# Optimization experiments

Hardware: AMD Instinct MI355X
Metric: run time of the kernel (lower is better)

Reference implementation:

```python
import jax, jax.numpy as jnp
import numpy as np
from jax import lax

NR, NC, DI, DO = 2048, 10, 8, 16  # routes, digit caps, in-dim, out-dim

# (t1, a1, b1, a2, b2, t3, a3, b3, a4, b4) piecewise-affine squash constants
PRIM_CONSTS = (-13.46416092, 0.000242759, 0.024488359, 0.002769205, 0.06089699,
               13.23405266, -0.002828244, 0.061313814, -0.000219038, 0.023874787)
DIGIT_CONSTS = (-0.075410217, -0.074520095, 0.349297946, -0.534473989, 0.27196494,
                0.062207676, 0.637642944, 0.295330779, 0.169344703, 0.353784456)


def _piecewise(s, t1, a1, b1, a2, b2, t3, a3, b3, a4, b4):
    # Faithful to the torch loop: new_sorted aliases sorted, so each segment
    # count (i1,i2,i3) is computed on the PARTIALLY-MODIFIED array, and each
    # slice end is idx-1 (off-by-one in the source), last slice ends at n-1.
    n = s.shape[0]
    ar = jnp.arange(n)
    i1 = jnp.sum(s < t1)
    s = jnp.where(ar < i1 - 1, a1 * s + b1, s)
    i2 = jnp.sum(s < 0.0)
    s = jnp.where((ar >= i1) & (ar < i2 - 1), a2 * s + b2, s)
    i3 = jnp.sum(s < t3)
    s = jnp.where((ar >= i2) & (ar < i3 - 1), a3 * s + b3, s)
    s = jnp.where((ar >= i3) & (ar < n - 1), a4 * s + b4, s)
    return s


def _squash_map(x, consts):
    # sort -> piecewise-affine remap -> unsort (one row)
    idx = jnp.argsort(x)
    s = _piecewise(x[idx], *consts)
    return s[jnp.argsort(idx)]


def _conv(x, w, b, stride):
    y = lax.conv_general_dilated(x, w, (stride, stride), 'VALID',
                                 dimension_numbers=('NCHW', 'OIHW', 'NCHW'))
    return y + b[None, :, None, None]


def capsnet_forward(data, conv1_w, conv1_b, prim_w, prim_b, W_dc,
                    dec_w1, dec_b1, dec_w2, dec_b2, dec_w3, dec_b3):
    B = data.shape[0]
    x = jax.nn.relu(_conv(data, conv1_w, conv1_b, 1))          # (B,256,24,24)
    u = _conv(x, prim_w, prim_b, 2).reshape(B, NR, DI)          # (B,2048,8) : 8 caps x 32ch x 8x8
    mag = jax.vmap(lambda r: _squash_map(r, PRIM_CONSTS))(u[:, :, 0])  # (B,2048)
    u_sq = mag[:, :, None] * u                                  # PrimaryCaps.my_squash2
    u_hat = jnp.einsum('rcoi,bri->brco', W_dc, u_sq)            # (B,2048,10,16)

    b_ij = jnp.zeros((NR, NC), dtype=u_hat.dtype)               # routing logits
    for it in range(3):
        c_ij = jax.nn.softmax(b_ij, axis=0)                     # softmax over routes (dim=1 in torch)
        s_j = jnp.einsum('rc,brco->bco', c_ij, u_hat)           # (B,10,16)
        f = jax.vmap(lambda r: _squash_map(r, DIGIT_CONSTS))(s_j[:, :, 0])  # (B,10)
        # torch writes the remapped value back into s_j in place (view aliasing),
        # so component 0 of v_j is f*f while other components are f*s_j
        s_mod = s_j.at[:, :, 0].set(f)
        v_j = f[:, :, None] * s_mod                             # (B,10,16)
        if it < 2:
            a_ij = jnp.einsum('brco,bco->brc', u_hat, v_j)      # agreement
            b_ij = b_ij + a_ij.mean(axis=0)

    # Decoder (reconstruction head)
    classes = jnp.sqrt(jnp.sum(v_j ** 2, axis=2))               # (B,10)
    classes = jax.nn.softmax(classes, axis=0)                   # softmax over batch, as in source
    idx = jnp.argmax(classes, axis=1)                           # (B,)
    masked = jnp.eye(NC, dtype=v_j.dtype)[idx]                  # (B,10) one-hot
    t = (v_j * masked[:, :, None]).reshape(B, -1)               # (B,160)
    h = jax.nn.relu(t @ dec_w1.T + dec_b1)
    h = jax.nn.relu(h @ dec_w2.T + dec_b2)
    recon = jax.nn.sigmoid(h @ dec_w3.T + dec_b3)               # (B,1024) = 32*32*1
    # single-array output: [flattened digit caps | flattened reconstruction]
    return jnp.concatenate([v_j.reshape(B, -1), recon], axis=1)  # (B,1184)


def setup_inputs() -> dict:
    key = jax.random.key(0)
    ks = jax.random.split(key, 12)
    f32 = jnp.float32
    return {
        'data': jax.random.normal(ks[0], (100, 1, 32, 32), f32),
        'conv1_w': jax.random.normal(ks[1], (256, 1, 9, 9), f32) * (1.0 / 9.0),
        'conv1_b': jnp.zeros((256,), f32),
        'prim_w': jax.random.normal(ks[2], (256, 256, 9, 9), f32) * (1.0 / 144.0),
        'prim_b': jnp.zeros((256,), f32),
        'W_dc': jax.random.normal(ks[3], (2048, 10, 16, 8), f32) * 0.05,
        'dec_w1': jax.random.normal(ks[4], (512, 160), f32) * 0.079,
        'dec_b1': jnp.zeros((512,), f32),
        'dec_w2': jax.random.normal(ks[5], (1024, 512), f32) * 0.0442,
        'dec_b2': jnp.zeros((1024,), f32),
        'dec_w3': jax.random.normal(ks[6], (1024, 1024), f32) * 0.03125,
        'dec_b3': jnp.zeros((1024,), f32),
        'train_or_test': 0,
        'epch': 0,
    }


def reference(data, conv1_w, conv1_b, prim_w, prim_b, W_dc,
              dec_w1, dec_b1, dec_w2, dec_b2, dec_w3, dec_b3,
              train_or_test, epch):
    return capsnet_forward(data, conv1_w, conv1_b, prim_w, prim_b, W_dc,
                           dec_w1, dec_b1, dec_w2, dec_b2, dec_w3, dec_b3)
```

## Files before the change

### kernel.cpp

```cpp
#include <hip/hip_runtime.h>
#include <cstdint>
#include <cstddef>


#define BATCH 100

static const size_t OFF_WT   = 0;
static const size_t OFF_X1   = 5308416;
static const size_t OFF_PU   = 20054016;
static const size_t OFF_UHAT = 0;
static const size_t OFF_U    = 33161216;
static const size_t OFF_BIJ  = 32768000;
static const size_t OFF_CIJ  = 32788480;
static const size_t OFF_SP   = 32808960;
static const size_t OFF_VJ   = 33064960;
static const size_t OFF_IDX  = 33080960;
static const size_t OFF_H1   = 33081088;
static const size_t OFF_H2   = 33132288;

#define PT1f -13.46416092f
#define PA1f 0.000242759f
#define PB1f 0.024488359f
#define PA2f 0.002769205f
#define PB2f 0.06089699f
#define PT3f 13.23405266f
#define PA3f -0.002828244f
#define PB3f 0.061313814f
#define PA4f -0.000219038f
#define PB4f 0.023874787f

#define DT1f -0.075410217f
#define DA1f -0.074520095f
#define DB1f 0.349297946f
#define DA2f -0.534473989f
#define DB2f 0.27196494f
#define DT3f 0.062207676f
#define DA3f 0.637642944f
#define DB3f 0.295330779f
#define DA4f 0.169344703f
#define DB4f 0.353784456f

__global__ __launch_bounds__(256)
void k_transpose_w(const float* __restrict__ w, float* __restrict__ wt) {
  __shared__ float tile[64 * 82];
  int ci = blockIdx.x, co0 = blockIdx.y * 64, t = threadIdx.x;
  for (int f = t; f < 64 * 81; f += 256) {
    int col = f / 81, tap = f - col * 81;
    tile[col * 82 + tap] = w[(size_t)(co0 + col) * 20736 + (size_t)ci * 81 + tap];
  }
  __syncthreads();
  for (int g = t; g < 64 * 81; g += 256) {
    int tap = g / 64, col = g - tap * 64;
    wt[((size_t)ci * 81 + tap) * 256 + co0 + col] = tile[col * 82 + tap];
  }
}

__global__ __launch_bounds__(256)
void k_conv1(const float* __restrict__ data, const float* __restrict__ cw,
             const float* __restrict__ cb, float* __restrict__ x1) {
  __shared__ float img[1024];
  __shared__ float wl[81 * 32];
  int b = blockIdx.x, cg = blockIdx.y, t = threadIdx.x;
  for (int f = t; f < 1024; f += 256) img[f] = data[(size_t)b * 1024 + f];
  for (int f = t; f < 2592; f += 256) {
    int tap = f >> 5, c = f & 31;
    wl[f] = cw[(size_t)(cg * 32 + c) * 81 + tap];
  }
  __syncthreads();
  for (int task = t; task < 1152; task += 256) {
    int q = task % 144, cq = task / 144;
    int p0 = q * 4, oh = p0 / 24, ow0 = p0 % 24;
    float a[4][4];
#pragma unroll
    for (int i = 0; i < 4; ++i)
#pragma unroll
      for (int j = 0; j < 4; ++j) a[i][j] = 0.f;
    for (int kh = 0; kh < 9; ++kh) {
      const float* ir = &img[(oh + kh) * 32 + ow0];
      const float* wr = &wl[kh * 9 * 32 + cq * 4];
#pragma unroll
      for (int kw = 0; kw < 9; ++kw) {
        float4 wv = *(const float4*)(wr + kw * 32);
#pragma unroll
        for (int j = 0; j < 4; ++j) {
          float xv = ir[kw + j];
          a[0][j] = fmaf(wv.x, xv, a[0][j]);
          a[1][j] = fmaf(wv.y, xv, a[1][j]);
          a[2][j] = fmaf(wv.z, xv, a[2][j]);
          a[3][j] = fmaf(wv.w, xv, a[3][j]);
        }
      }
    }
#pragma unroll
    for (int cc = 0; cc < 4; ++cc) {
      int c = cg * 32 + cq * 4 + cc;
      float bias = cb[c];
      float4 o4 = make_float4(fmaxf(a[cc][0] + bias, 0.f), fmaxf(a[cc][1] + bias, 0.f),
                              fmaxf(a[cc][2] + bias, 0.f), fmaxf(a[cc][3] + bias, 0.f));
      *(float4*)&x1[((size_t)(b * 256 + c) * 24 + oh) * 24 + ow0] = o4;
    }
  }
}

__global__ __launch_bounds__(256, 5)
void k_prim(const float* __restrict__ x1, const float* __restrict__ wt,
            float* __restrict__ pu) {
  __shared__ float wsh[81 * 32];
  __shared__ float xsh[4 * 2 * 288];
  int t = threadIdx.x;
  int tb = t >> 6, tl = t & 63;
  int coq = tl >> 3, oh = tl & 7;
  int ci_base = blockIdx.x * 32, cog = blockIdx.y, bq = blockIdx.z;
  int b = bq * 4 + tb;

  float acc[4][8];
#pragma unroll
  for (int i = 0; i < 4; ++i)
#pragma unroll
    for (int j = 0; j < 8; ++j) acc[i][j] = 0.f;

#pragma unroll 1
  for (int ci = ci_base; ci < ci_base + 32; ++ci) {
    __syncthreads();
    for (int f = t; f < 288; f += 256) {
      int tbj = f / 72, rem = f - tbj * 72;
      int r = rem / 3, oct = rem - r * 3;
      const float* gp = &x1[((size_t)(bq * 4 + tbj) * 256 + ci) * 576 + r * 24 + oct * 8];
      float4 v1 = *(const float4*)gp;
      float4 v2 = *(const float4*)(gp + 4);
      float* eb = &xsh[tbj * 576 + r * 12 + oct * 4];
      *(float4*)eb = make_float4(v1.x, v1.z, v2.x, v2.z);
      *(float4*)(eb + 288) = make_float4(v1.y, v1.w, v2.y, v2.w);
    }
    for (int f = t; f < 648; f += 256) {
      int tap = f >> 3, cq = f & 7;
      float4 v = *(const float4*)&wt[((size_t)ci * 81 + tap) * 256 + cog * 32 + cq * 4];
      *(float4*)&wsh[tap * 32 + cq * 4] = v;
    }
    __syncthreads();
    const float* xb = &xsh[tb * 576];
    const float* wb = &wsh[coq * 4];
#pragma unroll 3
    for (int kh = 0; kh < 9; ++kh) {
      int r = 2 * oh + kh;
      const float* xe = xb + r * 12;
      float ew[12], ov[12];
      *(float4*)&ew[0] = *(const float4*)xe;
      *(float4*)&ew[4] = *(const float4*)(xe + 4);
      *(float4*)&ew[8] = *(const float4*)(xe + 8);
      *(float4*)&ov[0] = *(const float4*)(xe + 288);
      *(float4*)&ov[4] = *(const float4*)(xe + 292);
      *(float4*)&ov[8] = *(const float4*)(xe + 296);
      const float* wr = wb + kh * 9 * 32;
#pragma unroll
      for (int p = 0; p < 5; ++p) {
        float4 wv = *(const float4*)(wr + p * 64);
#pragma unroll
        for (int j = 0; j < 8; ++j) {
          float xv = ew[p + j];
          acc[0][j] = fmaf(wv.x, xv, acc[0][j]);
          acc[1][j] = fmaf(wv.y, xv, acc[1][j]);
          acc[2][j] = fmaf(wv.z, xv, acc[2][j]);
          acc[3][j] = fmaf(wv.w, xv, acc[3][j]);
        }
      }
#pragma unroll
      for (int p = 0; p < 4; ++p) {
        float4 wv = *(const float4*)(wr + 32 + p * 64);
#pragma unroll
        for (int j = 0; j < 8; ++j) {
          float xv = ov[p + j];
          acc[0][j] = fmaf(wv.x, xv, acc[0][j]);
          acc[1][j] = fmaf(wv.y, xv, acc[1][j]);
          acc[2][j] = fmaf(wv.z, xv, acc[2][j]);
          acc[3][j] = fmaf(wv.w, xv, acc[3][j]);
        }
      }
    }
  }
  float* pp = pu + (((size_t)blockIdx.x * BATCH + b) * 2048 +
                    (cog * 32 + coq * 4) * 8 + oh) * 8;
#pragma unroll
  for (int cc = 0; cc < 4; ++cc) {
    *(float4*)(pp + cc * 64)     = make_float4(acc[cc][0], acc[cc][1], acc[cc][2], acc[cc][3]);
    *(float4*)(pp + cc * 64 + 4) = make_float4(acc[cc][4], acc[cc][5], acc[cc][6], acc[cc][7]);
  }
}

__global__ __launch_bounds__(256)
void k_ured(const float* __restrict__ pu, const float* __restrict__ pb,
            float* __restrict__ u) {
  int g4 = blockIdx.x * 256 + threadIdx.x;
  if (g4 >= 409600) return;
  size_t g = (size_t)g4 * 4;
  const size_t S = 1638400;
  float4 s = *(const float4*)(pu + g);
#pragma unroll
  for (int k = 1; k < 8; ++k) {
    float4 p = *(const float4*)(pu + (size_t)k * S + g);
    s.x += p.x; s.y += p.y; s.z += p.z; s.w += p.w;
  }
  int r = (int)((g >> 3) & 2047);
  float bias = pb[r >> 3];
  float4 o = make_float4(s.x + bias, s.y + bias, s.z + bias, s.w + bias);
  *(float4*)(u + g) = o;
}

__global__ __launch_bounds__(256)
void k_squash(float* __restrict__ u) {
  __shared__ float kv[2048];
  __shared__ int kid[2048];
  __shared__ int red[256];
  int b = blockIdx.x, t = threadIdx.x;
  for (int r = t; r < 2048; r += 256) {
    kv[r] = u[((size_t)b * 2048 + r) * 8];
    kid[r] = r;
  }
  __syncthreads();
  for (int size = 2; size <= 2048; size <<= 1) {
    for (int stride = size >> 1; stride > 0; stride >>= 1) {
#pragma unroll 1
      for (int s = 0; s < 4; ++s) {
        int i = t + s * 256;
        int pos = 2 * i - (i & (stride - 1));
        int q = pos + stride;
        float va = kv[pos], vb = kv[q];
        int ia = kid[pos], ib = kid[q];
        bool gt = (va > vb) || (va == vb && ia > ib);
        bool up = ((pos & size) == 0);
        if (gt == up) { kv[pos] = vb; kv[q] = va; kid[pos] = ib; kid[q] = ia; }
      }
      __syncthreads();
    }
  }
  int loc = 0;
#pragma unroll
  for (int s = 0; s < 8; ++s) loc += (kv[t + s * 256] < PT1f) ? 1 : 0;
  red[t] = loc; __syncthreads();
  for (int off = 128; off; off >>= 1) { if (t < off) red[t] += red[t + off]; __syncthreads(); }
  int i1 = red[0]; __syncthreads();
  float m1v[8];
  loc = 0;
#pragma unroll
  for (int s = 0; s < 8; ++s) {
    int p = t + s * 256;
    float v = kv[p];
    float m = (p < i1 - 1) ? (PA1f * v + PB1f) : v;
    m1v[s] = m;
    loc += (m < 0.f) ? 1 : 0;
  }
  red[t] = loc; __syncthreads();
  for (int off = 128; off; off >>= 1) { if (t < off) red[t] += red[t + off]; __syncthreads(); }
  int i2 = red[0]; __syncthreads();
  float m2v[8];
  loc = 0;
#pragma unroll
  for (int s = 0; s < 8; ++s) {
    int p = t + s * 256;
    float m = (p >= i1 && p < i2 - 1) ? (PA2f * m1v[s] + PB2f) : m1v[s];
    m2v[s] = m;
    loc += (m < PT3f) ? 1 : 0;
  }
  red[t] = loc; __syncthreads();
  for (int off = 128; off; off >>= 1) { if (t < off) red[t] += red[t + off]; __syncthreads(); }
  int i3 = red[0]; __syncthreads();
#pragma unroll
  for (int s = 0; s < 8; ++s) {
    int p = t + s * 256;
    float m = m2v[s];
    m = (p >= i2 && p < i3 - 1) ? (PA3f * m + PB3f) : m;
    m = (p >= i3 && p < 2047) ? (PA4f * m + PB4f) : m;
    int rid = kid[p];
    float* row = u + ((size_t)b * 2048 + rid) * 8;
    float4 lo = *(float4*)row;
    float4 hi = *(float4*)(row + 4);
    lo.x *= m; lo.y *= m; lo.z *= m; lo.w *= m;
    hi.x *= m; hi.y *= m; hi.z *= m; hi.w *= m;
    *(float4*)row = lo;
    *(float4*)(row + 4) = hi;
  }
}

__global__ __launch_bounds__(192)
void k_uhat(const float* __restrict__ Wdc, const float* __restrict__ usq,
            float* __restrict__ uhat) {
  int t = threadIdx.x;
  if (t >= 160) return;
  int r0 = blockIdx.x * 8;
  for (int rl = 0; rl < 8; ++rl) {
    int r = r0 + rl;
    const float* wp = Wdc + ((size_t)r * 160 + t) * 8;
    float4 wa = *(const float4*)wp;
    float4 wb = *(const float4*)(wp + 4);
#pragma unroll 2
    for (int b = 0; b < BATCH; ++b) {
      const float* us = usq + ((size_t)b * 2048 + r) * 8;
      float v = us[0] * wa.x + us[1] * wa.y + us[2] * wa.z + us[3] * wa.w +
                us[4] * wb.x + us[5] * wb.y + us[6] * wb.z + us[7] * wb.w;
      uhat[((size_t)b * 2048 + r) * 160 + t] = v;
    }
  }
}

__global__ __launch_bounds__(256)
void k_softc(const float* __restrict__ bij, float* __restrict__ cij) {
  __shared__ float red[256];
  int c = blockIdx.x, t = threadIdx.x;
  float m = -3.402823466e38f;
  for (int r = t; r < 2048; r += 256) m = fmaxf(m, bij[r * 10 + c]);
  red[t] = m; __syncthreads();
  for (int off = 128; off; off >>= 1) { if (t < off) red[t] = fmaxf(red[t], red[t + off]); __syncthreads(); }
  m = red[0]; __syncthreads();
  float s = 0.f;
  for (int r = t; r < 2048; r += 256) s += expf(bij[r * 10 + c] - m);
  red[t] = s; __syncthreads();
  for (int off = 128; off; off >>= 1) { if (t < off) red[t] += red[t + off]; __syncthreads(); }
  s = red[0];
  for (int r = t; r < 2048; r += 256) cij[r * 10 + c] = expf(bij[r * 10 + c] - m) / s;
}

__global__ __launch_bounds__(192)
void k_sjpart(const float* __restrict__ cij, const float* __restrict__ uhat,
              float* __restrict__ sp, int it0) {
  __shared__ float cl[1280];
  int b = blockIdx.x, ch = blockIdx.y, t = threadIdx.x;
  if (!it0) {
    for (int f = t; f < 1280; f += 192) cl[f] = cij[(size_t)ch * 1280 + f];
  }
  __syncthreads();
  if (t < 160) {
    int c = t >> 4;
    float acc = 0.f;
    const float* up = uhat + ((size_t)b * 2048 + ch * 128) * 160 + t;
    if (it0) {
      const float cuni = 0.00048828125f;
#pragma unroll 4
      for (int rl = 0; rl < 128; ++rl) acc += cuni * up[(size_t)rl * 160];
    } else {
#pragma unroll 4
      for (int rl = 0; rl < 128; ++rl) acc += cl[rl * 10 + c] * up[(size_t)rl * 160];
    }
    sp[((size_t)b * 16 + ch) * 160 + t] = acc;
  }
}

__global__ __launch_bounds__(192)
void k_sjred(const float* __restrict__ sp, float* __restrict__ vj,
             float* __restrict__ dout, int finalit) {
  __shared__ float sl[160];
  __shared__ float fl[10];
  int b = blockIdx.x, t = threadIdx.x;
  if (t < 160) {
    float a = 0.f;
#pragma unroll
    for (int ch = 0; ch < 16; ++ch) a += sp[((size_t)b * 16 + ch) * 160 + t];
    sl[t] = a;
  }
  __syncthreads();
  if (t == 0) {
    float sv[10]; int rk[10];
    for (int c = 0; c < 10; ++c) sv[c] = sl[c * 16];
    for (int c = 0; c < 10; ++c) {
      int r = 0;
      for (int k = 0; k < 10; ++k)
        r += ((sv[k] < sv[c]) || (sv[k] == sv[c] && k < c)) ? 1 : 0;
      rk[c] = r;
    }
    int i1 = 0;
    for (int c = 0; c < 10; ++c) i1 += (sv[c] < DT1f) ? 1 : 0;
    float m1[10];
    for (int c = 0; c < 10; ++c) m1[c] = (rk[c] < i1 - 1) ? (DA1f * sv[c] + DB1f) : sv[c];
    int i2 = 0;
    for (int c = 0; c < 10; ++c) i2 += (m1[c] < 0.f) ? 1 : 0;
    float m2[10];
    for (int c = 0; c < 10; ++c)
      m2[c] = (rk[c] >= i1 && rk[c] < i2 - 1) ? (DA2f * m1[c] + DB2f) : m1[c];
    int i3 = 0;
    for (int c = 0; c < 10; ++c) i3 += (m2[c] < DT3f) ? 1 : 0;
    for (int c = 0; c < 10; ++c) {
      float m = (rk[c] >= i2 && rk[c] < i3 - 1) ? (DA3f * m2[c] + DB3f) : m2[c];
      m = (rk[c] >= i3 && rk[c] < 9) ? (DA4f * m + DB4f) : m;
      fl[c] = m;
    }
  }
  __syncthreads();
  if (t < 160) {
    int c = t >> 4, o = t & 15;
    float fv = fl[c];
    float v = fv * ((o == 0) ? fv : sl[t]);
    vj[(size_t)b * 160 + t] = v;
    if (finalit) dout[(size_t)b * 1184 + t] = v;
  }
}

__global__ __launch_bounds__(192)
void k_amean(const float* __restrict__ uhat, const float* __restrict__ vj,
             float* __restrict__ bij, int first) {
  __shared__ float vl[16000];
  int t = threadIdx.x, r0 = blockIdx.x * 8;
  for (int f = t; f < 16000; f += 192) vl[f] = vj[f];
  __syncthreads();
  if (t < 160) {
    int c = t >> 4;
    for (int rl = 0; rl < 8; ++rl) {
      int r = r0 + rl;
      float acc = 0.f;
      const float* up = uhat + (size_t)r * 160 + t;
#pragma unroll 4
      for (int b = 0; b < BATCH; ++b) acc += up[(size_t)b * 2048 * 160] * vl[b * 160 + t];
      for (int off = 8; off; off >>= 1) acc += __shfl_down(acc, off, 16);
      if ((t & 15) == 0) {
        float val = acc / 100.0f;
        bij[r * 10 + c] = first ? val : (bij[r * 10 + c] + val);
      }
    }
  }
}

__global__ __launch_bounds__(256)
void k_cls(const float* __restrict__ vj, int* __restrict__ idxg) {
  __shared__ float cl[1000];
  __shared__ float cm[10];
  __shared__ float cs[10];
  int t = threadIdx.x;
  for (int f = t; f < 1000; f += 256) {
    int b = f / 10, c = f - b * 10;
    float s = 0.f;
#pragma unroll
    for (int o = 0; o < 16; ++o) {
      float v = vj[(size_t)b * 160 + c * 16 + o];
      s += v * v;
    }
    cl[f] = sqrtf(s);
  }
  __syncthreads();
  if (t < 10) {
    float m = -3.402823466e38f;
    for (int b = 0; b < BATCH; ++b) m = fmaxf(m, cl[b * 10 + t]);
    float s = 0.f;
    for (int b = 0; b < BATCH; ++b) s += expf(cl[b * 10 + t] - m);
    cm[t] = m; cs[t] = s;
  }
  __syncthreads();
  for (int b = t; b < BATCH; b += 256) {
    float best = -1.f; int bi = 0;
    for (int c = 0; c < 10; ++c) {
      float val = expf(cl[b * 10 + c] - cm[c]) / cs[c];
      if (val > best) { best = val; bi = c; }
    }
    idxg[b] = bi;
  }
}

__global__ __launch_bounds__(256)
void k_dec1(const float* __restrict__ w1, const float* __restrict__ b1,
            const float* __restrict__ vj, const int* __restrict__ idxg,
            float* __restrict__ h1) {
  int b = blockIdx.x, t = threadIdx.x;
  int id = idxg[b];
  const float* v = vj + (size_t)b * 160 + id * 16;
  for (int j = t; j < 512; j += 256) {
    float acc = b1[j];
    const float* wr = w1 + (size_t)j * 160 + id * 16;
#pragma unroll
    for (int o = 0; o < 16; ++o) acc += wr[o] * v[o];
    h1[(size_t)b * 512 + j] = fmaxf(acc, 0.f);
  }
}

__global__ __launch_bounds__(256)
void k_dec2(const float* __restrict__ w2, const float* __restrict__ b2,
            const float* __restrict__ h1, float* __restrict__ h2) {
  __shared__ float red[4][64][4];
  int t = threadIdx.x, lane = t & 63, strip = t >> 6;
  int j = blockIdx.x * 64 + lane, bs = blockIdx.y * 4;
  float acc[4] = {0.f, 0.f, 0.f, 0.f};
  const float* wr = w2 + (size_t)j * 512 + strip * 128;
  const float* hb = h1 + (size_t)bs * 512 + strip * 128;
  for (int k4 = 0; k4 < 32; ++k4) {
    float4 wv = *(const float4*)(wr + k4 * 4);
    const float* h0 = hb + k4 * 4;
#pragma unroll
    for (int q = 0; q < 4; ++q) {
      float4 hv = *(const float4*)(h0 + q * 512);
      acc[q] += wv.x * hv.x + wv.y * hv.y + wv.z * hv.z + wv.w * hv.w;
    }
  }
#pragma unroll
  for (int q = 0; q < 4; ++q) red[strip][lane][q] = acc[q];
  __syncthreads();
  if (strip == 0) {
    float bias = b2[j];
#pragma unroll
    for (int q = 0; q < 4; ++q) {
      float tot = red[0][lane][q] + red[1][lane][q] + red[2][lane][q] + red[3][lane][q] + bias;
      h2[(size_t)(bs + q) * 1024 + j] = fmaxf(tot, 0.f);
    }
  }
}

__global__ __launch_bounds__(256)
void k_dec3(const float* __restrict__ w3, const float* __restrict__ b3,
            const float* __restrict__ h2, float* __restrict__ dout) {
  __shared__ float red[4][64][4];
  int t = threadIdx.x, lane = t & 63, strip = t >> 6;
  int j = blockIdx.x * 64 + lane, bs = blockIdx.y * 4;
  float acc[4] = {0.f, 0.f, 0.f, 0.f};
  const float* wr = w3 + (size_t)j * 1024 + strip * 256;
  const float* hb = h2 + (size_t)bs * 1024 + strip * 256;
  for (int k4 = 0; k4 < 64; ++k4) {
    float4 wv = *(const float4*)(wr + k4 * 4);
    const float* h0 = hb + k4 * 4;
#pragma unroll
    for (int q = 0; q < 4; ++q) {
      float4 hv = *(const float4*)(h0 + q * 1024);
      acc[q] += wv.x * hv.x + wv.y * hv.y + wv.z * hv.z + wv.w * hv.w;
    }
  }
#pragma unroll
  for (int q = 0; q < 4; ++q) red[strip][lane][q] = acc[q];
  __syncthreads();
  if (strip == 0) {
    float bias = b3[j];
#pragma unroll
    for (int q = 0; q < 4; ++q) {
      float tot = red[0][lane][q] + red[1][lane][q] + red[2][lane][q] + red[3][lane][q] + bias;
      dout[(size_t)(bs + q) * 1184 + 160 + j] = 1.f / (1.f + expf(-tot));
    }
  }
}

extern "C" void kernel_launch(void* const* d_in, const int* in_sizes, int n_in,
                              void* d_out, int out_size, void* d_ws, size_t ws_size,
                              hipStream_t stream) {
  (void)in_sizes; (void)n_in; (void)out_size; (void)ws_size;
  const float* data = (const float*)d_in[0];
  const float* c1w  = (const float*)d_in[1];
  const float* c1b  = (const float*)d_in[2];
  const float* pw   = (const float*)d_in[3];
  const float* pb   = (const float*)d_in[4];
  const float* Wdc  = (const float*)d_in[5];
  const float* w1   = (const float*)d_in[6];
  const float* b1   = (const float*)d_in[7];
  const float* w2   = (const float*)d_in[8];
  const float* b2   = (const float*)d_in[9];
  const float* w3   = (const float*)d_in[10];
  const float* b3   = (const float*)d_in[11];
  float* out = (float*)d_out;
  float* ws  = (float*)d_ws;

  float* WT   = ws + OFF_WT;
  float* X1   = ws + OFF_X1;
  float* PU   = ws + OFF_PU;
  float* UHAT = ws + OFF_UHAT;
  float* U    = ws + OFF_U;
  float* BIJ  = ws + OFF_BIJ;
  float* CIJ  = ws + OFF_CIJ;
  float* SP   = ws + OFF_SP;
  float* VJ   = ws + OFF_VJ;
  int*   IDX  = (int*)(ws + OFF_IDX);
  float* H1   = ws + OFF_H1;
  float* H2   = ws + OFF_H2;

  k_transpose_w<<<dim3(256, 4), 256, 0, stream>>>(pw, WT);
  k_conv1<<<dim3(BATCH, 8), 256, 0, stream>>>(data, c1w, c1b, X1);
  k_prim<<<dim3(8, 8, 25), 256, 0, stream>>>(X1, WT, PU);
  k_ured<<<1600, 256, 0, stream>>>(PU, pb, U);
  k_squash<<<BATCH, 256, 0, stream>>>(U);
  k_uhat<<<256, 192, 0, stream>>>(Wdc, U, UHAT);

  for (int it = 0; it < 3; ++it) {
    if (it > 0) k_softc<<<10, 256, 0, stream>>>(BIJ, CIJ);
    k_sjpart<<<dim3(BATCH, 16), 192, 0, stream>>>(CIJ, UHAT, SP, it == 0 ? 1 : 0);
    k_sjred<<<BATCH, 192, 0, stream>>>(SP, VJ, out, it == 2 ? 1 : 0);
    if (it < 2) k_amean<<<256, 192, 0, stream>>>(UHAT, VJ, BIJ, it == 0 ? 1 : 0);
  }

  k_cls<<<1, 256, 0, stream>>>(VJ, IDX);
  k_dec1<<<BATCH, 256, 0, stream>>>(w1, b1, VJ, IDX, H1);
  k_dec2<<<dim3(16, 25), 256, 0, stream>>>(w2, b2, H1, H2);
  k_dec3<<<dim3(16, 25), 256, 0, stream>>>(w3, b3, H2, out);
}
```

Measured before the change: 1.460 ms.

## Pad prim conv shared rows, batch routes in uhat and agreement kernels

The primary-capsule conv pads its shared-memory input rows (an extra 4 floats every two rows, with a new phase offset) to reduce LDS bank conflicts, and raises the launch-bounds occupancy hint from 5 to 8 blocks. The u_hat kernel now loads weights for 4 routes at once and processes them together inside the batch loop. The agreement kernel interchanges its loops so 8 route accumulators advance together per batch element, giving more independent loads in flight. The higher occupancy hint may force register spills in the conv kernel.

```diff
diff --git a/kernel.cpp b/kernel.cpp
--- a/kernel.cpp
+++ b/kernel.cpp
@@ -40,6 +40,10 @@
 #define DA4f 0.169344703f
 #define DB4f 0.353784456f
 
+#define XROW(r) ((r) * 12 + ((r) >> 1) * 4)
+#define XPH 332
+#define XTB 664
+
 __global__ __launch_bounds__(256)
 void k_transpose_w(const float* __restrict__ w, float* __restrict__ wt) {
   __shared__ float tile[64 * 82];
@@ -102,11 +106,11 @@
   }
 }
 
-__global__ __launch_bounds__(256, 5)
+__global__ __launch_bounds__(256, 8)
 void k_prim(const float* __restrict__ x1, const float* __restrict__ wt,
             float* __restrict__ pu) {
   __shared__ float wsh[81 * 32];
-  __shared__ float xsh[4 * 2 * 288];
+  __shared__ float xsh[4 * XTB];
   int t = threadIdx.x;
   int tb = t >> 6, tl = t & 63;
   int coq = tl >> 3, oh = tl & 7;
@@ -128,9 +132,9 @@
       const float* gp = &x1[((size_t)(bq * 4 + tbj) * 256 + ci) * 576 + r * 24 + oct * 8];
       float4 v1 = *(const float4*)gp;
       float4 v2 = *(const float4*)(gp + 4);
-      float* eb = &xsh[tbj * 576 + r * 12 + oct * 4];
+      float* eb = &xsh[tbj * XTB + XROW(r) + oct * 4];
       *(float4*)eb = make_float4(v1.x, v1.z, v2.x, v2.z);
-      *(float4*)(eb + 288) = make_float4(v1.y, v1.w, v2.y, v2.w);
+      *(float4*)(eb + XPH) = make_float4(v1.y, v1.w, v2.y, v2.w);
     }
     for (int f = t; f < 648; f += 256) {
       int tap = f >> 3, cq = f & 7;
@@ -138,19 +142,19 @@
       *(float4*)&wsh[tap * 32 + cq * 4] = v;
     }
     __syncthreads();
-    const float* xb = &xsh[tb * 576];
+    const float* xb = &xsh[tb * XTB];
     const float* wb = &wsh[coq * 4];
 #pragma unroll 3
     for (int kh = 0; kh < 9; ++kh) {
       int r = 2 * oh + kh;
-      const float* xe = xb + r * 12;
+      const float* xe = xb + XROW(r);
       float ew[12], ov[12];
       *(float4*)&ew[0] = *(const float4*)xe;
       *(float4*)&ew[4] = *(const float4*)(xe + 4);
       *(float4*)&ew[8] = *(const float4*)(xe + 8);
-      *(float4*)&ov[0] = *(const float4*)(xe + 288);
-      *(float4*)&ov[4] = *(const float4*)(xe + 292);
-      *(float4*)&ov[8] = *(const float4*)(xe + 296);
+      *(float4*)&ov[0] = *(const float4*)(xe + XPH);
+      *(float4*)&ov[4] = *(const float4*)(xe + XPH + 4);
+      *(float4*)&ov[8] = *(const float4*)(xe + XPH + 8);
       const float* wr = wb + kh * 9 * 32;
 #pragma unroll
       for (int p = 0; p < 5; ++p) {
@@ -287,17 +291,27 @@
   int t = threadIdx.x;
   if (t >= 160) return;
   int r0 = blockIdx.x * 8;
-  for (int rl = 0; rl < 8; ++rl) {
-    int r = r0 + rl;
-    const float* wp = Wdc + ((size_t)r * 160 + t) * 8;
-    float4 wa = *(const float4*)wp;
-    float4 wb = *(const float4*)(wp + 4);
+#pragma unroll 1
+  for (int half = 0; half < 2; ++half) {
+    int rb = r0 + half * 4;
+    float4 wa[4], wb4[4];
+#pragma unroll
+    for (int rl = 0; rl < 4; ++rl) {
+      const float* wp = Wdc + ((size_t)(rb + rl) * 160 + t) * 8;
+      wa[rl]  = *(const float4*)wp;
+      wb4[rl] = *(const float4*)(wp + 4);
+    }
 #pragma unroll 2
     for (int b = 0; b < BATCH; ++b) {
-      const float* us = usq + ((size_t)b * 2048 + r) * 8;
-      float v = us[0] * wa.x + us[1] * wa.y + us[2] * wa.z + us[3] * wa.w +
-                us[4] * wb.x + us[5] * wb.y + us[6] * wb.z + us[7] * wb.w;
-      uhat[((size_t)b * 2048 + r) * 160 + t] = v;
+      const float* ub = usq + ((size_t)b * 2048 + rb) * 8;
+      float* op = uhat + ((size_t)b * 2048 + rb) * 160 + t;
+#pragma unroll
+      for (int rl = 0; rl < 4; ++rl) {
+        const float* us = ub + rl * 8;
+        float v = us[0] * wa[rl].x + us[1] * wa[rl].y + us[2] * wa[rl].z + us[3] * wa[rl].w +
+                  us[4] * wb4[rl].x + us[5] * wb4[rl].y + us[6] * wb4[rl].z + us[7] * wb4[rl].w;
+        op[(size_t)rl * 160] = v;
+      }
     }
   }
 }
@@ -402,15 +416,25 @@
   __syncthreads();
   if (t < 160) {
     int c = t >> 4;
+    float acc[8];
+#pragma unroll
+    for (int rl = 0; rl < 8; ++rl) acc[rl] = 0.f;
+    const float* up0 = uhat + (size_t)r0 * 160 + t;
+#pragma unroll 2
+    for (int b = 0; b < BATCH; ++b) {
+      float vv = vl[b * 160 + t];
+      const float* up = up0 + (size_t)b * 327680;
+#pragma unroll
+      for (int rl = 0; rl < 8; ++rl)
+        acc[rl] = fmaf(up[(size_t)rl * 160], vv, acc[rl]);
+    }
+#pragma unroll
     for (int rl = 0; rl < 8; ++rl) {
-      int r = r0 + rl;
-      float acc = 0.f;
-      const float* up = uhat + (size_t)r * 160 + t;
-#pragma unroll 4
-      for (int b = 0; b < BATCH; ++b) acc += up[(size_t)b * 2048 * 160] * vl[b * 160 + t];
-      for (int off = 8; off; off >>= 1) acc += __shfl_down(acc, off, 16);
+      float a = acc[rl];
+      for (int off = 8; off; off >>= 1) a += __shfl_down(a, off, 16);
       if ((t & 15) == 0) {
-        float val = acc / 100.0f;
+        int r = r0 + rl;
+        float val = a / 100.0f;
         bij[r * 10 + c] = first ? val : (bij[r * 10 + c] + val);
       }
     }
```

Measured after the change: 1.290 ms. 11.6% less time.
